# Performance work log

Measured on AMD Instinct MI355X. Metric: run time of the kernel, lower is better.

Reference implementation:

```python
import jax, jax.numpy as jnp
import numpy as np
import math

DIM = 2048
N_HEADS = 32
N_KV_HEADS = 8
HEAD_DIM = DIM // N_HEADS  # 64
N_REP = N_HEADS // N_KV_HEADS
B, S = 2, 2048


def _rope(x, cos, sin):
    # x: [B, S, H, Hd]; cos/sin: [S, Hd//2]
    xr = x[..., 0::2]
    xi = x[..., 1::2]
    c = cos[None, :, None, :]
    s = sin[None, :, None, :]
    or_ = xr * c - xi * s
    oi_ = xr * s + xi * c
    return jnp.stack([or_, oi_], axis=-1).reshape(x.shape)


def setup_inputs() -> dict:
    key = jax.random.key(0)
    ks = jax.random.split(key, 8)
    x = jax.random.normal(ks[0], (B, S, DIM), dtype=jnp.float32)
    # standard RoPE frequency tables
    inv_freq = 1.0 / (10000.0 ** (np.arange(0, HEAD_DIM, 2, dtype=np.float32) / HEAD_DIM))
    t = np.arange(S, dtype=np.float32)
    freqs = np.outer(t, inv_freq)  # [S, HEAD_DIM//2]
    freqs_cos = jnp.asarray(np.cos(freqs))
    freqs_sin = jnp.asarray(np.sin(freqs))
    attn_mask = jnp.zeros((S, S), dtype=jnp.float32)
    sc = 0.02
    wq = jax.random.normal(ks[1], (DIM, N_HEADS * HEAD_DIM), dtype=jnp.float32) * sc
    wk = jax.random.normal(ks[2], (DIM, N_KV_HEADS * HEAD_DIM), dtype=jnp.float32) * sc
    wv = jax.random.normal(ks[3], (DIM, N_KV_HEADS * HEAD_DIM), dtype=jnp.float32) * sc
    wo = jax.random.normal(ks[4], (DIM, DIM), dtype=jnp.float32) * sc
    return {"x": x, "freqs_cos": freqs_cos, "freqs_sin": freqs_sin,
            "attn_mask": attn_mask, "wq": wq, "wk": wk, "wv": wv, "wo": wo}


def reference(x, freqs_cos, freqs_sin, attn_mask, wq, wk, wv, wo):
    bsz, seqlen, _ = x.shape
    xq = (x @ wq).reshape(bsz, seqlen, N_HEADS, HEAD_DIM)
    xk = (x @ wk).reshape(bsz, seqlen, N_KV_HEADS, HEAD_DIM)
    xv = (x @ wv).reshape(bsz, seqlen, N_KV_HEADS, HEAD_DIM)
    xq = _rope(xq, freqs_cos, freqs_sin)
    xk = _rope(xk, freqs_cos, freqs_sin)
    # GQA repeat: [B,S,Hkv,Hd] -> [B,S,H,Hd]
    xk = jnp.repeat(xk, N_REP, axis=2)
    xv = jnp.repeat(xv, N_REP, axis=2)
    xq = xq.swapaxes(1, 2)  # [B,H,S,Hd]
    xk = xk.swapaxes(1, 2)
    xv = xv.swapaxes(1, 2)
    scores = jnp.einsum('bhqd,bhkd->bhqk', xq, xk) / math.sqrt(HEAD_DIM)
    scores = scores + attn_mask[None, None, :seqlen, :seqlen]
    probs = jax.nn.softmax(scores, axis=-1)
    out = jnp.einsum('bhqk,bhkd->bhqd', probs, xv)
    out = out.swapaxes(1, 2).reshape(bsz, seqlen, -1)
    return out @ wo
```

## Files before the change

### kernel.cpp

```cpp
#include <hip/hip_runtime.h>

typedef unsigned short u16;
typedef __bf16 bf16x8 __attribute__((ext_vector_type(8)));
typedef float f32x4 __attribute__((ext_vector_type(4)));
typedef float f32x16 __attribute__((ext_vector_type(16)));
typedef unsigned short u16x4 __attribute__((ext_vector_type(4)));
typedef unsigned int u32x4 __attribute__((ext_vector_type(4)));

typedef __attribute__((address_space(1))) const unsigned int* gas_t;
typedef __attribute__((address_space(3))) unsigned int* las_t;

__device__ __forceinline__ void gload16(const void* gsrc, void* ldst) {
  __builtin_amdgcn_global_load_lds((gas_t)gsrc, (las_t)ldst, 16, 0, 0);
}

__device__ __forceinline__ u16 f2bf(float f) {
  unsigned u = __builtin_bit_cast(unsigned, f);
  unsigned r = u + 0x7fffu + ((u >> 16) & 1u);
  return (u16)(r >> 16);
}
__device__ __forceinline__ float bf2f(u16 h) {
  unsigned u = ((unsigned)h) << 16;
  return __builtin_bit_cast(float, u);
}
__device__ __forceinline__ unsigned cvtpk(float lo, float hi) {
  unsigned r;
  asm("v_cvt_pk_bf16_f32 %0, %1, %2" : "=v"(r) : "v"(lo), "v"(hi));
  return r;
}
__device__ __forceinline__ float fexp2(float x) {
  return __builtin_amdgcn_exp2f(x);
}

#define QSCALE 0.1803368801111204f
#define L2E    1.44269504088896f

__global__ __launch_bounds__(256) void cvt_x(const float* __restrict__ x, u16* __restrict__ xb) {
  int i = blockIdx.x * 256 + threadIdx.x;
  f32x4 v = ((const f32x4*)x)[i];
  u16x4 o = { f2bf(v[0]), f2bf(v[1]), f2bf(v[2]), f2bf(v[3]) };
  ((u16x4*)xb)[i] = o;
}

__global__ __launch_bounds__(256) void transpose_cvt(const float* __restrict__ in, u16* __restrict__ out,
                                                     int K, int N) {
  __shared__ float tile[32][33];
  int n0 = blockIdx.x * 32, k0 = blockIdx.y * 32;
  int tx = threadIdx.x, ty = threadIdx.y;
#pragma unroll
  for (int i = 0; i < 4; ++i)
    tile[ty + i * 8][tx] = in[(size_t)(k0 + ty + i * 8) * N + n0 + tx];
  __syncthreads();
#pragma unroll
  for (int i = 0; i < 4; ++i)
    out[(size_t)(n0 + ty + i * 8) * K + k0 + tx] = f2bf(tile[tx][ty + i * 8]);
}

template <int OUTBF>
__global__ __launch_bounds__(256) void gemm_bt(const u16* __restrict__ A, const u16* __restrict__ Bt,
                                               void* __restrict__ Cout, int M, int N, int K) {
  __shared__ u16 As[128 * 64];
  __shared__ u16 Bs[128 * 64];
  const int tid = threadIdx.x;
  const int w = tid >> 6, l = tid & 63, lg = l >> 4, lr = l & 15;
  const int m0 = blockIdx.y * 128, n0 = blockIdx.x * 128;
  const int wr = w >> 1, wc = w & 1;

  size_t srcA[4], srcB[4];
  int ldst[4];
#pragma unroll
  for (int j = 0; j < 4; ++j) {
    int c = j * 256 + tid;
    int row = c >> 3, kb = (c & 7) ^ (row & 7);
    srcA[j] = (size_t)(m0 + row) * K + kb * 8;
    srcB[j] = (size_t)(n0 + row) * K + kb * 8;
    ldst[j] = (j * 256 + w * 64) * 8;
  }

  const int lx = lr & 7;
  int aoff[2][4], boff[2][4];
#pragma unroll
  for (int kk = 0; kk < 2; ++kk) {
#pragma unroll
    for (int m = 0; m < 4; ++m)
      aoff[kk][m] = (wr * 64 + m * 16 + lr) * 128 + ((((kk << 2) | lg) ^ lx) << 4);
#pragma unroll
    for (int n = 0; n < 4; ++n)
      boff[kk][n] = (wc * 64 + n * 16 + lr) * 128 + ((((kk << 2) | lg) ^ lx) << 4);
  }

  f32x4 acc[4][4];
#pragma unroll
  for (int m = 0; m < 4; ++m)
#pragma unroll
    for (int n = 0; n < 4; ++n) acc[m][n] = (f32x4){0.f, 0.f, 0.f, 0.f};

  for (int k0 = 0; k0 < K; k0 += 64) {
    __syncthreads();
#pragma unroll
    for (int j = 0; j < 4; ++j) {
      gload16(A + k0 + srcA[j], &As[ldst[j]]);
      gload16(Bt + k0 + srcB[j], &Bs[ldst[j]]);
    }
    __syncthreads();
#pragma unroll
    for (int kk = 0; kk < 2; ++kk) {
      bf16x8 af[4], bf[4];
#pragma unroll
      for (int m = 0; m < 4; ++m)
        af[m] = *(const bf16x8*)((const char*)As + aoff[kk][m]);
#pragma unroll
      for (int n = 0; n < 4; ++n)
        bf[n] = *(const bf16x8*)((const char*)Bs + boff[kk][n]);
      __builtin_amdgcn_s_setprio(1);
#pragma unroll
      for (int m = 0; m < 4; ++m)
#pragma unroll
        for (int n = 0; n < 4; ++n)
          acc[m][n] = __builtin_amdgcn_mfma_f32_16x16x32_bf16(af[m], bf[n], acc[m][n], 0, 0, 0);
      __builtin_amdgcn_s_setprio(0);
    }
  }
#pragma unroll
  for (int m = 0; m < 4; ++m)
#pragma unroll
    for (int n = 0; n < 4; ++n)
#pragma unroll
      for (int r = 0; r < 4; ++r) {
        int row = m0 + wr * 64 + m * 16 + lg * 4 + r;
        int col = n0 + wc * 64 + n * 16 + lr;
        float v = acc[m][n][r];
        if (OUTBF)
          ((u16*)Cout)[(size_t)row * N + col] = f2bf(v);
        else
          ((float*)Cout)[(size_t)row * N + col] = v;
      }
}

__global__ __launch_bounds__(256) void rope_kernel(const u16* __restrict__ qkv, const float* __restrict__ fcos,
                                                   const float* __restrict__ fsin, u16* __restrict__ dst,
                                                   int nhs , int col0, float scale) {
  int idx = blockIdx.x * 256 + threadIdx.x;
  int p = idx & 31;
  int h = (idx >> 5) & ((1 << nhs) - 1);
  int t = idx >> (5 + nhs);
  int s = t & 2047, b = t >> 11;
  unsigned v = *(const unsigned*)(qkv + (size_t)t * 3072 + col0 + h * 64 + 2 * p);
  float xr = bf2f((u16)(v & 0xffff)), xi = bf2f((u16)(v >> 16));
  float c = fcos[s * 32 + p], sn = fsin[s * 32 + p];
  float orr = (xr * c - xi * sn) * scale;
  float oii = (xr * sn + xi * c) * scale;
  unsigned o = (unsigned)f2bf(orr) | ((unsigned)f2bf(oii) << 16);
  *(unsigned*)(dst + (((size_t)((b << nhs) + h) * 2048 + s) * 64 + 2 * p)) = o;
}

__global__ __launch_bounds__(256) void vtrans(const u16* __restrict__ qkv, u16* __restrict__ vT) {
  __shared__ u16 tile[32][33];
  int c0 = blockIdx.x * 32, t0 = blockIdx.y * 32;
  int tx = threadIdx.x, ty = threadIdx.y;
#pragma unroll
  for (int i = 0; i < 4; ++i)
    tile[ty + i * 8][tx] = qkv[(size_t)(t0 + ty + i * 8) * 3072 + 2560 + c0 + tx];
  __syncthreads();
#pragma unroll
  for (int i = 0; i < 4; ++i) {
    int c = c0 + ty + i * 8;
    int tok = t0 + tx;
    int ts = (tok & ~15) | (tok & 3) | ((tok & 4) << 1) | ((tok & 8) >> 1);
    vT[((size_t)((tok >> 11) * 8 + (c >> 6)) * 64 + (c & 63)) * 2048 + (ts & 2047)] = tile[tx][ty + i * 8];
  }
}

__global__ __launch_bounds__(256) void mask_flags(const float* __restrict__ mask, unsigned* __restrict__ Fl) {
  int qt = blockIdx.x, kt = blockIdx.y;
  int t = threadIdx.x;
  int row = qt * 128 + (t >> 1);
  const f32x4* p = (const f32x4*)(mask + (size_t)row * 2048 + kt * 64 + (t & 1) * 32);
  bool any = false;
#pragma unroll
  for (int j = 0; j < 8; ++j) {
    f32x4 v = p[j];
    any |= (v[0] != 0.f) | (v[1] != 0.f) | (v[2] != 0.f) | (v[3] != 0.f);
  }
  if (__any(any) && (t & 63) == 0) atomicOr(&Fl[qt], 1u << kt);
}

__global__ __launch_bounds__(256, 4) void attn(const u16* __restrict__ QKVraw,
                                               const float* __restrict__ fcos, const float* __restrict__ fsin,
                                               const u16* __restrict__ Kb, const u16* __restrict__ Vt,
                                               const float* __restrict__ mask,
                                               const unsigned* __restrict__ Fl, u16* __restrict__ Ao) {
  __shared__ u16 Ks[2][4096];
  __shared__ u16 Vs[2][4096];
  const int bid = blockIdx.x;
  const int qt = bid & 15, h = (bid >> 4) & 31, b = bid >> 9;
  const int kv = h >> 2;
  const int tid = threadIdx.x, w = tid >> 6, l = tid & 63;
  const int lq = l & 31, hi = l >> 5;

  const int srowq = qt * 128 + w * 32 + lq;
  const u16* Qb = QKVraw + (size_t)(b * 2048 + srowq) * 3072 + h * 64;
  bf16x8 qf[4];
#pragma unroll
  for (int t = 0; t < 4; ++t) {
    bf16x8 qr = *(const bf16x8*)(Qb + t * 16 + hi * 8);
    u32x4 qw = __builtin_bit_cast(u32x4, qr);
    f32x4 cc = *(const f32x4*)(fcos + srowq * 32 + t * 8 + hi * 4);
    f32x4 ss = *(const f32x4*)(fsin + srowq * 32 + t * 8 + hi * 4);
    u32x4 ow;
#pragma unroll
    for (int j = 0; j < 4; ++j) {
      unsigned wrd = qw[j];
      float xr = bf2f((u16)(wrd & 0xffff)), xi = bf2f((u16)(wrd >> 16));
      float orr = (xr * cc[j] - xi * ss[j]) * QSCALE;
      float oii = (xr * ss[j] + xi * cc[j]) * QSCALE;
      ow[j] = cvtpk(orr, oii);
    }
    qf[t] = __builtin_bit_cast(bf16x8, ow);
  }

  const u16* Ksrc = Kb + (size_t)(b * 8 + kv) * 2048 * 64;
  const u16* Vsrc = Vt + (size_t)(b * 8 + kv) * 64 * 2048;
  const float* Mrow = mask + (size_t)srowq * 2048;
  const unsigned flagbits = Fl[qt];

  const int lx = lq & 7;
  int koff[8];
#pragma unroll
  for (int ks = 0; ks < 2; ++ks)
#pragma unroll
    for (int t = 0; t < 4; ++t)
      koff[ks * 4 + t] = (lq + 32 * ks) * 128 + ((((t << 1) + hi) ^ lx) << 4);
  int voff[8];
#pragma unroll
  for (int ks = 0; ks < 2; ++ks)
#pragma unroll
    for (int t = 0; t < 2; ++t)
#pragma unroll
      for (int dblk = 0; dblk < 2; ++dblk)
        voff[(ks * 2 + t) * 2 + dblk] =
            (lq + 32 * dblk) * 128 + ((((ks << 2) + (t << 1) + hi) ^ lx) << 4);

  size_t kgoff[2], vgoff[2];
  int ldso[2];
#pragma unroll
  for (int j = 0; j < 2; ++j) {
    int c = w * 64 + j * 256 + l;
    int row = c >> 3;
    int sc_ = ((c & 7) ^ (row & 7)) * 8;
    kgoff[j] = (size_t)row * 64 + sc_;
    vgoff[j] = (size_t)row * 2048 + sc_;
    ldso[j] = (w * 64 + j * 256) * 8;
  }

  f32x16 o0, o1, zacc;
#pragma unroll
  for (int i = 0; i < 16; ++i) { o0[i] = 0.f; o1[i] = 0.f; zacc[i] = 0.f; }
  float mrun2 = 0.f, lrun = 0.f;

  auto stage = [&](int kt2, int bu2) {
#pragma unroll
    for (int j = 0; j < 2; ++j) {
      gload16(Ksrc + (size_t)kt2 * 4096 + kgoff[j], &Ks[bu2][ldso[j]]);
      gload16(Vsrc + (size_t)kt2 * 64 + vgoff[j], &Vs[bu2][ldso[j]]);
    }
  };

  stage(0, 0);
  __syncthreads();

  for (int kt = 0; kt < 32; ++kt) {
    const int bu = kt & 1;
    if (kt < 31) stage(kt + 1, bu ^ 1);
    const char* KL = (const char*)Ks[bu];
    const char* VL = (const char*)Vs[bu];
    const bool havemask = (flagbits >> kt) & 1;

#pragma unroll
    for (int ks = 0; ks < 2; ++ks) {
      __builtin_amdgcn_s_setprio(1);
      bf16x8 kf = *(const bf16x8*)(KL + koff[ks * 4]);
      f32x16 a = __builtin_amdgcn_mfma_f32_32x32x16_bf16(kf, qf[0], zacc, 0, 0, 0);
#pragma unroll
      for (int t = 1; t < 4; ++t) {
        kf = *(const bf16x8*)(KL + koff[ks * 4 + t]);
        a = __builtin_amdgcn_mfma_f32_32x32x16_bf16(kf, qf[t], a, 0, 0, 0);
      }
      __builtin_amdgcn_s_setprio(0);

      if (havemask) {
#pragma unroll
        for (int g = 0; g < 4; ++g) {
          f32x4 mk = *(const f32x4*)(Mrow + kt * 64 + ks * 32 + g * 8 + hi * 4);
#pragma unroll
          for (int i = 0; i < 4; ++i) a[g * 4 + i] = fmaf(mk[i], L2E, a[g * 4 + i]);
        }
      }

      float ps0 = 0.f, ps1 = 0.f, ps2 = 0.f, ps3 = 0.f;
      if (mrun2 == 0.f) {
#pragma unroll
        for (int i = 0; i < 16; i += 4) {
          float p0 = fexp2(a[i]);
          float p1 = fexp2(a[i + 1]);
          float p2 = fexp2(a[i + 2]);
          float p3 = fexp2(a[i + 3]);
          a[i] = p0; a[i + 1] = p1; a[i + 2] = p2; a[i + 3] = p3;
          ps0 += p0; ps1 += p1; ps2 += p2; ps3 += p3;
        }
      } else {
#pragma unroll
        for (int i = 0; i < 16; i += 4) {
          float p0 = fexp2(a[i] - mrun2);
          float p1 = fexp2(a[i + 1] - mrun2);
          float p2 = fexp2(a[i + 2] - mrun2);
          float p3 = fexp2(a[i + 3] - mrun2);
          a[i] = p0; a[i + 1] = p1; a[i + 2] = p2; a[i + 3] = p3;
          ps0 += p0; ps1 += p1; ps2 += p2; ps3 += p3;
        }
      }
      lrun += (ps0 + ps1) + (ps2 + ps3);

      unsigned uu0 = cvtpk(a[0], a[1]);
      unsigned uu1 = cvtpk(a[2], a[3]);
      unsigned uu2 = cvtpk(a[4], a[5]);
      unsigned uu3 = cvtpk(a[6], a[7]);
      unsigned uu4 = cvtpk(a[8], a[9]);
      unsigned uu5 = cvtpk(a[10], a[11]);
      unsigned uu6 = cvtpk(a[12], a[13]);
      unsigned uu7 = cvtpk(a[14], a[15]);
      __builtin_amdgcn_s_setprio(1);
#pragma unroll
      for (int t = 0; t < 2; ++t) {
        u32x4 wv_;
        if (t == 0) wv_ = (u32x4){uu0, uu1, uu2, uu3};
        else        wv_ = (u32x4){uu4, uu5, uu6, uu7};
        bf16x8 pa = __builtin_bit_cast(bf16x8, wv_);
#pragma unroll
        for (int dblk = 0; dblk < 2; ++dblk) {
          bf16x8 vfrag = *(const bf16x8*)(VL + voff[(ks * 2 + t) * 2 + dblk]);
          if (dblk == 0) o0 = __builtin_amdgcn_mfma_f32_32x32x16_bf16(pa, vfrag, o0, 0, 0, 0);
          else           o1 = __builtin_amdgcn_mfma_f32_32x32x16_bf16(pa, vfrag, o1, 0, 0, 0);
        }
      }
      __builtin_amdgcn_s_setprio(0);
    }

    if (__builtin_expect(__any(lrun > 1.0e27f), 0)) {
      const float DS = 5.421010862427522e-20f;
      mrun2 += 64.0f;
      lrun *= DS;
#pragma unroll
      for (int r = 0; r < 16; ++r) { o0[r] *= DS; o1[r] *= DS; }
    }

    __syncthreads();
  }

  lrun += __shfl_xor(lrun, 32);
  float linv = 1.0f / lrun;
#pragma unroll
  for (int r = 0; r < 16; ++r) {
    int oq = (r & 3) + 8 * (r >> 2) + 4 * hi;
    float inv = __shfl(linv, oq);
    int srow = qt * 128 + w * 32 + oq;
    size_t tok = (size_t)(b * 2048 + srow);
    Ao[tok * 2048 + h * 64 + lq]      = f2bf(o0[r] * inv);
    Ao[tok * 2048 + h * 64 + 32 + lq] = f2bf(o1[r] * inv);
  }
}

extern "C" void kernel_launch(void* const* d_in, const int* in_sizes, int n_in,
                              void* d_out, int out_size, void* d_ws, size_t ws_size,
                              hipStream_t stream) {
  const float* x    = (const float*)d_in[0];
  const float* fcos = (const float*)d_in[1];
  const float* fsin = (const float*)d_in[2];
  const float* mask = (const float*)d_in[3];
  const float* wq   = (const float*)d_in[4];
  const float* wk   = (const float*)d_in[5];
  const float* wv   = (const float*)d_in[6];
  const float* wo   = (const float*)d_in[7];
  float* out = (float*)d_out;

  u16* ws  = (u16*)d_ws;
  u16* xb  = ws;
  u16* wT  = ws + 8388608;
  u16* qkv = ws + 14680064;
  u16* kb  = ws + 35651584;
  u16* vT  = ws + 37748736;
  unsigned* Fl = (unsigned*)(ws + 27262976);

  cvt_x<<<8192, 256, 0, stream>>>(x, xb);
  transpose_cvt<<<dim3(64, 64), dim3(32, 8), 0, stream>>>(wq, wT, 2048, 2048);
  transpose_cvt<<<dim3(16, 64), dim3(32, 8), 0, stream>>>(wk, wT + (size_t)2048 * 2048, 2048, 512);
  transpose_cvt<<<dim3(16, 64), dim3(32, 8), 0, stream>>>(wv, wT + (size_t)2560 * 2048, 2048, 512);
  gemm_bt<1><<<dim3(24, 32), 256, 0, stream>>>(xb, wT, qkv, 4096, 3072, 2048);
  transpose_cvt<<<dim3(64, 64), dim3(32, 8), 0, stream>>>(wo, wT, 2048, 2048);
  rope_kernel<<<4096, 256, 0, stream>>>(qkv, fcos, fsin, kb, 3, 2048, 1.0f);
  vtrans<<<dim3(16, 128), dim3(32, 8), 0, stream>>>(qkv, vT);
  hipMemsetAsync(Fl, 0, 16 * sizeof(unsigned), stream);
  mask_flags<<<dim3(16, 32), 256, 0, stream>>>(mask, Fl);
  attn<<<1024, 256, 0, stream>>>(qkv, fcos, fsin, kb, vT, mask, Fl, xb);
  gemm_bt<0><<<dim3(16, 32), 256, 0, stream>>>(xb, wT, out, 4096, 2048, 2048);
}
```

Measured before the change: 220.1 us.

## Single-buffer V tile and raise attention occupancy to six blocks per CU

The V shared-memory tile goes from double to single buffering, which cuts LDS per block so the launch bound can be raised from 4 to 6 blocks per CU. V for the current tile is now issued at the start of each iteration, and a new barrier between the QK/softmax phase and the PV phase makes it visible before use. The rescale check moves before that barrier. The packed probabilities for both k-subtiles are kept in registers across the barrier. This trades the V prefetch overlap and an extra barrier per iteration for more resident waves, and the tighter launch bound may force register spills.

```diff
diff --git a/kernel.cpp b/kernel.cpp
--- a/kernel.cpp
+++ b/kernel.cpp
@@ -185,13 +185,13 @@
   if (__any(any) && (t & 63) == 0) atomicOr(&Fl[qt], 1u << kt);
 }
 
-__global__ __launch_bounds__(256, 4) void attn(const u16* __restrict__ QKVraw,
+__global__ __launch_bounds__(256, 6) void attn(const u16* __restrict__ QKVraw,
                                                const float* __restrict__ fcos, const float* __restrict__ fsin,
                                                const u16* __restrict__ Kb, const u16* __restrict__ Vt,
                                                const float* __restrict__ mask,
                                                const unsigned* __restrict__ Fl, u16* __restrict__ Ao) {
   __shared__ u16 Ks[2][4096];
-  __shared__ u16 Vs[2][4096];
+  __shared__ u16 Vs[4096];
   const int bid = blockIdx.x;
   const int qt = bid & 15, h = (bid >> 4) & 31, b = bid >> 9;
   const int kv = h >> 2;
@@ -258,24 +258,29 @@
   for (int i = 0; i < 16; ++i) { o0[i] = 0.f; o1[i] = 0.f; zacc[i] = 0.f; }
   float mrun2 = 0.f, lrun = 0.f;
 
-  auto stage = [&](int kt2, int bu2) {
-#pragma unroll
-    for (int j = 0; j < 2; ++j) {
-      gload16(Ksrc + (size_t)kt2 * 4096 + kgoff[j], &Ks[bu2][ldso[j]]);
-      gload16(Vsrc + (size_t)kt2 * 64 + vgoff[j], &Vs[bu2][ldso[j]]);
-    }
+  auto stageK = [&](int kt2) {
+#pragma unroll
+    for (int j = 0; j < 2; ++j)
+      gload16(Ksrc + (size_t)kt2 * 4096 + kgoff[j], &Ks[kt2 & 1][ldso[j]]);
   };
-
-  stage(0, 0);
+  auto stageV = [&](int kt2) {
+#pragma unroll
+    for (int j = 0; j < 2; ++j)
+      gload16(Vsrc + (size_t)kt2 * 64 + vgoff[j], &Vs[ldso[j]]);
+  };
+
+  stageK(0);
   __syncthreads();
 
   for (int kt = 0; kt < 32; ++kt) {
     const int bu = kt & 1;
-    if (kt < 31) stage(kt + 1, bu ^ 1);
+    stageV(kt);
+    if (kt < 31) stageK(kt + 1);
     const char* KL = (const char*)Ks[bu];
-    const char* VL = (const char*)Vs[bu];
+    const char* VL = (const char*)Vs;
     const bool havemask = (flagbits >> kt) & 1;
 
+    unsigned pw[2][8];
 #pragma unroll
     for (int ks = 0; ks < 2; ++ks) {
       __builtin_amdgcn_s_setprio(1);
@@ -321,20 +326,32 @@
       }
       lrun += (ps0 + ps1) + (ps2 + ps3);
 
-      unsigned uu0 = cvtpk(a[0], a[1]);
-      unsigned uu1 = cvtpk(a[2], a[3]);
-      unsigned uu2 = cvtpk(a[4], a[5]);
-      unsigned uu3 = cvtpk(a[6], a[7]);
-      unsigned uu4 = cvtpk(a[8], a[9]);
-      unsigned uu5 = cvtpk(a[10], a[11]);
-      unsigned uu6 = cvtpk(a[12], a[13]);
-      unsigned uu7 = cvtpk(a[14], a[15]);
+      pw[ks][0] = cvtpk(a[0], a[1]);
+      pw[ks][1] = cvtpk(a[2], a[3]);
+      pw[ks][2] = cvtpk(a[4], a[5]);
+      pw[ks][3] = cvtpk(a[6], a[7]);
+      pw[ks][4] = cvtpk(a[8], a[9]);
+      pw[ks][5] = cvtpk(a[10], a[11]);
+      pw[ks][6] = cvtpk(a[12], a[13]);
+      pw[ks][7] = cvtpk(a[14], a[15]);
+    }
+
+    if (__builtin_expect(__any(lrun > 1.0e27f), 0)) {
+      const float DS = 5.421010862427522e-20f;
+      mrun2 += 64.0f;
+      lrun *= DS;
+#pragma unroll
+      for (int r = 0; r < 16; ++r) { o0[r] *= DS; o1[r] *= DS; }
+    }
+
+    __syncthreads();
+
+#pragma unroll
+    for (int ks = 0; ks < 2; ++ks) {
       __builtin_amdgcn_s_setprio(1);
 #pragma unroll
       for (int t = 0; t < 2; ++t) {
-        u32x4 wv_;
-        if (t == 0) wv_ = (u32x4){uu0, uu1, uu2, uu3};
-        else        wv_ = (u32x4){uu4, uu5, uu6, uu7};
+        u32x4 wv_ = (u32x4){pw[ks][t * 4 + 0], pw[ks][t * 4 + 1], pw[ks][t * 4 + 2], pw[ks][t * 4 + 3]};
         bf16x8 pa = __builtin_bit_cast(bf16x8, wv_);
 #pragma unroll
         for (int dblk = 0; dblk < 2; ++dblk) {
@@ -344,14 +361,6 @@
         }
       }
       __builtin_amdgcn_s_setprio(0);
-    }
-
-    if (__builtin_expect(__any(lrun > 1.0e27f), 0)) {
-      const float DS = 5.421010862427522e-20f;
-      mrun2 += 64.0f;
-      lrun *= DS;
-#pragma unroll
-      for (int r = 0; r < 16; ++r) { o0[r] *= DS; o1[r] *= DS; }
     }
 
     __syncthreads();
```

Result: slower. 456.4 us (+107.3%).
